# Performance work log

Hardware: AMD Instinct MI355X
Metric: run time of the kernel (lower is better)

## Reference

```python
import jax, jax.numpy as jnp
import numpy as np
from jax.scipy.special import gammaln

NPTS = 100          # hardcoded npts default in the torch module
EPS = 1e-8          # self.epsilon


def _build_grid(K):
    # Static quadrature grids for thresholds t_i = i/K, i=0..K.
    # Original code builds torch.linspace(eps, t_i - eps, int(NPTS * t_i)) per bin;
    # we precompute all K+1 grids padded to NPTS points with a validity mask.
    # (Note: the repo's thresholds arange/K*2-1 in [-1,1] crash torch.linspace for
    # negative b; we use the intended [0,1] Beta support thresholds t_i = i/K.)
    grid = np.full((K + 1, NPTS), 0.5, dtype=np.float32)  # 0.5 pad avoids log(0)
    mask = np.zeros((K + 1, NPTS), dtype=np.float32)
    for i in range(K + 1):
        n = int(NPTS * (i / K))
        if n > 0:
            grid[i, :n] = np.linspace(EPS, i / K - EPS, n, dtype=np.float32)
            mask[i, :n] = 1.0
    return jnp.asarray(grid), jnp.asarray(mask)


def setup_inputs() -> dict:
    key = jax.random.key(0)
    k1, k2, k3 = jax.random.split(key, 3)
    B, C, K = 65536, 512, 10
    x = jax.random.normal(k1, (B, C), dtype=jnp.float32)
    Wa = jax.random.normal(k2, (C, 1), dtype=jnp.float32) / np.sqrt(C)
    ba = jnp.zeros((1,), dtype=jnp.float32)
    Wb = jax.random.normal(k3, (C, 1), dtype=jnp.float32) / np.sqrt(C)
    bb = jnp.zeros((1,), dtype=jnp.float32)
    return {"x": x, "Wa": Wa, "ba": ba, "Wb": Wb, "bb": bb, "num_classes": K}


def reference(x, Wa, ba, Wb, bb, num_classes):
    K = int(num_classes)
    grid, mask = _build_grid(K)                      # [K+1, NPTS]
    # alpha/beta heads: Linear -> Softplus -> 1 + . -> clamp(1, 100)
    alpha = jnp.clip(1.0 + jax.nn.softplus(x @ Wa + ba), 1.0, 100.0)  # [B, 1]
    beta = jnp.clip(1.0 + jax.nn.softplus(x @ Wb + bb), 1.0, 100.0)   # [B, 1]
    a = alpha[:, :, None]                            # [B, 1, 1]
    b = beta[:, :, None]
    # Beta log_prob on all quadrature points: [B, K+1, NPTS]
    log_norm = gammaln(a) + gammaln(b) - gammaln(a + b)
    logpdf = (a - 1.0) * jnp.log(grid) + (b - 1.0) * jnp.log1p(-grid) - log_norm
    dx = 1.0 / (NPTS * K)                            # dx constant from original code
    cdf = jnp.sum(jnp.exp(logpdf) * mask, axis=-1) * dx   # [B, K+1] unnormalized CDFs
    probs = cdf[:, 1:] - cdf[:, :-1]                 # per-bin mass, [B, K]
    # diag(1/rowsum) @ probs  ==  row-normalize
    return probs / jnp.sum(probs, axis=-1, keepdims=True)
```

## Files before the change

kernel.cpp:

```cpp
#include <hip/hip_runtime.h>
#include <math.h>

#define NPTS_C 100
#define EPS_C 1e-8

#if defined(__has_builtin)
# if __has_builtin(__builtin_amdgcn_exp2f)
#  define FAST_EXP2(x) __builtin_amdgcn_exp2f(x)
#  define FAST_LOG2(x) __builtin_amdgcn_logf(x)
# else
#  define FAST_EXP2(x) exp2f(x)
#  define FAST_LOG2(x) log2f(x)
# endif
#else
# define FAST_EXP2(x) exp2f(x)
# define FAST_LOG2(x) log2f(x)
#endif

#define LOG2E_F 1.44269504088896340736f
#define LN2_F   0.69314718055994530942f

__device__ __forceinline__ float dot4(float4 a, float4 b) {
    return a.x * b.x + a.y * b.y + a.z * b.z + a.w * b.w;
}

__device__ __forceinline__ float wave_reduce_sum(float v) {
#pragma unroll
    for (int m = 1; m < 64; m <<= 1)
        v += __shfl_xor(v, m, 64);
    return v;
}

constexpr int KC   = 10;
constexpr int NTAB = 550;

__global__ __launch_bounds__(256, 6) void fused512_kernel(
    const float* __restrict__ x, const float* __restrict__ Wa,
    const float* __restrict__ ba, const float* __restrict__ Wb,
    const float* __restrict__ bb, float* __restrict__ out)
{
    __shared__ __align__(16) float2 s_tab[NTAB];
    __shared__ __align__(16) float4 s_w4[256];

    const int tid = threadIdx.x;

    if (tid < 128) {
        s_w4[tid]       = reinterpret_cast<const float4*>(Wa)[tid];
        s_w4[128 + tid] = reinterpret_cast<const float4*>(Wb)[tid];
    }

    {
        int base = 0;
#pragma unroll
        for (int i = 1; i <= KC; ++i) {
            const int n = 10 * i;
            const double start = EPS_C;
            const double stop  = (double)i / (double)KC - EPS_C;
            const double step  = (stop - start) / (double)(n - 1);
            for (int j = tid; j < n; j += 256) {
                const double g = (j == n - 1) ? stop : start + step * (double)j;
                const float g32 = (float)g;
                s_tab[base + j] = make_float2(log2f(g32), log2f(1.0f - g32));
            }
            base += n;
        }
    }
    __syncthreads();

    const int lane = tid & 63;
    const int wv   = tid >> 6;
    const int r8   = lane & 7;
    const int part = lane >> 3;
    const float ba0 = ba[0], bb0 = bb[0];

    const int row = blockIdx.x * 32 + wv * 8 + r8;
    const float* px = x + (size_t)row * 512 + part * 4;

    float da = 0.f, db = 0.f, da2 = 0.f, db2 = 0.f;
#pragma unroll
    for (int j = 0; j < 16; j += 2) {
        const float4 x0 = *reinterpret_cast<const float4*>(px + (size_t)j * 32);
        const float4 x1 = *reinterpret_cast<const float4*>(px + (size_t)(j + 1) * 32);
        da  += dot4(x0, s_w4[part + 8 * j]);
        db  += dot4(x0, s_w4[128 + part + 8 * j]);
        da2 += dot4(x1, s_w4[part + 8 * (j + 1)]);
        db2 += dot4(x1, s_w4[128 + part + 8 * (j + 1)]);
    }
    da += da2; db += db2;

    da += __shfl_xor(da, 8, 64);  db += __shfl_xor(db, 8, 64);
    da += __shfl_xor(da, 16, 64); db += __shfl_xor(db, 16, 64);
    da += __shfl_xor(da, 32, 64); db += __shfl_xor(db, 32, 64);
    da += ba0; db += bb0;

    const float ua = FAST_EXP2(-fabsf(da) * LOG2E_F);
    const float ub = FAST_EXP2(-fabsf(db) * LOG2E_F);
    const float sa = fmaxf(da, 0.f) + FAST_LOG2(1.f + ua) * LN2_F;
    const float sb = fmaxf(db, 0.f) + FAST_LOG2(1.f + ub) * LN2_F;
    const float alpha = fminf(fmaxf(1.f + sa, 1.f), 100.f);
    const float beta  = fminf(fmaxf(1.f + sb, 1.f), 100.f);
    const float am1 = alpha - 1.f, bm1 = beta - 1.f;

    const float den = am1 + bm1;
    float mm = (den > 0.f) ? am1 / den : 0.5f;
    mm = fminf(fmaxf(mm, 1e-6f), 1.f - 1e-6f);
    const float M2 = am1 * FAST_LOG2(mm) + bm1 * FAST_LOG2(1.f - mm);

    float seg[KC];
    {
        int base = 0;
#pragma unroll
        for (int i = 1; i <= KC; ++i) {
            const int n = 10 * i;
            float s = 0.f;
#pragma unroll
            for (int t = part; t < n; t += 8) {
                const float2 e = s_tab[base + t];
                s += FAST_EXP2(fmaf(am1, e.x, fmaf(bm1, e.y, -M2)));
            }
            seg[i - 1] = s;
            base += n;
        }
    }
#pragma unroll
    for (int i = 0; i < KC; ++i) {
        seg[i] += __shfl_xor(seg[i], 8, 64);
        seg[i] += __shfl_xor(seg[i], 16, 64);
        seg[i] += __shfl_xor(seg[i], 32, 64);
    }

    if (part == 0) {
        float* orow = out + (size_t)row * KC;
        const float inv_total = 1.f / seg[KC - 1];
        float prev = 0.f;
        float2* o2 = reinterpret_cast<float2*>(orow);
#pragma unroll
        for (int j = 0; j < KC; j += 2) {
            const float p0 = (seg[j]     - prev)   * inv_total;
            const float p1 = (seg[j + 1] - seg[j]) * inv_total;
            o2[j >> 1] = make_float2(p0, p1);
            prev = seg[j + 1];
        }
    }
}

__global__ __launch_bounds__(256, 4) void ub_fused_kernel(
    const float* __restrict__ x, const float* __restrict__ Wa,
    const float* __restrict__ ba, const float* __restrict__ Wb,
    const float* __restrict__ bb, float* __restrict__ out,
    int B, int C, int K)
{
    __shared__ __align__(16) float s_lg[600];
    __shared__ __align__(16) float s_l1g[600];
    __shared__ __align__(16) float s_w[1024];

    const int tid = threadIdx.x;
    for (int c = tid; c < C; c += blockDim.x) {
        s_w[c]     = Wa[c];
        s_w[C + c] = Wb[c];
    }
    {
        int base = 0;
        for (int i = 1; i <= K; ++i) {
            const int n = (int)((double)NPTS_C * ((double)i / (double)K));
            const double start = EPS_C;
            const double stop  = (double)i / (double)K - EPS_C;
            const double step  = (n > 1) ? (stop - start) / (double)(n - 1) : 0.0;
            for (int j = tid; j < n; j += blockDim.x) {
                float g = (j == n - 1) ? (float)stop : (float)(start + step * (double)j);
                s_lg[base + j]  = logf(g);
                s_l1g[base + j] = log1pf(-g);
            }
            base += n;
        }
    }
    __syncthreads();

    const float ba0 = ba[0], bb0 = bb[0];
    const int wave = tid >> 6;
    const int lane = tid & 63;
    const int wavesPerBlock = blockDim.x >> 6;
    const int waveId = blockIdx.x * wavesPerBlock + wave;
    const int nWaves = gridDim.x * wavesPerBlock;

    for (int row = waveId; row < B; row += nWaves) {
        const float* xr = x + (size_t)row * C;
        float da = 0.f, db = 0.f;
        for (int c0 = 0; c0 < C; c0 += 256) {
            const float4 xv = *reinterpret_cast<const float4*>(xr + c0 + 4 * lane);
            const float4 wa = *reinterpret_cast<const float4*>(&s_w[c0 + 4 * lane]);
            const float4 wb = *reinterpret_cast<const float4*>(&s_w[C + c0 + 4 * lane]);
            da += xv.x * wa.x + xv.y * wa.y + xv.z * wa.z + xv.w * wa.w;
            db += xv.x * wb.x + xv.y * wb.y + xv.z * wb.z + xv.w * wb.w;
        }
        da = wave_reduce_sum(da) + ba0;
        db = wave_reduce_sum(db) + bb0;

        const float sa = fmaxf(da, 0.f) + log1pf(expf(-fabsf(da)));
        const float sb = fmaxf(db, 0.f) + log1pf(expf(-fabsf(db)));
        const float alpha = fminf(fmaxf(1.f + sa, 1.f), 100.f);
        const float beta  = fminf(fmaxf(1.f + sb, 1.f), 100.f);
        const float log_norm = lgammaf(alpha) + lgammaf(beta) - lgammaf(alpha + beta);
        const float am1 = alpha - 1.f, bm1 = beta - 1.f;

        float cdf_prev = 0.f, myp = 0.f;
        int base = 0;
        for (int i = 1; i <= K; ++i) {
            const int n = (int)((double)NPTS_C * ((double)i / (double)K));
            float s = 0.f;
            for (int p = lane; p < n; p += 64) {
                const float lp = fmaf(am1, s_lg[base + p],
                                 fmaf(bm1, s_l1g[base + p], -log_norm));
                s += expf(lp);
            }
            const float cdf = wave_reduce_sum(s);
            if (lane == i - 1) myp = cdf - cdf_prev;
            cdf_prev = cdf;
            base += n;
        }
        if (lane < K)
            out[(size_t)row * K + lane] = myp / cdf_prev;
    }
}

extern "C" void kernel_launch(void* const* d_in, const int* in_sizes, int n_in,
                              void* d_out, int out_size, void* d_ws, size_t ws_size,
                              hipStream_t stream) {
    const float* x  = (const float*)d_in[0];
    const float* Wa = (const float*)d_in[1];
    const float* ba = (const float*)d_in[2];
    const float* Wb = (const float*)d_in[3];
    const float* bb = (const float*)d_in[4];
    float* out = (float*)d_out;

    const int C = in_sizes[1];
    const int B = in_sizes[0] / C;
    const int K = out_size / B;

    const bool fast_ok = (C == 512) && (K == 10) && (B % 32 == 0);

    if (fast_ok) {
        fused512_kernel<<<B / 32, 256, 0, stream>>>(x, Wa, ba, Wb, bb, out);
    } else {
        int nblocks = (B + 3) / 4;
        if (nblocks > 2048) nblocks = 2048;
        ub_fused_kernel<<<nblocks, 256, 0, stream>>>(x, Wa, ba, Wb, bb, out, B, C, K);
    }
}
```

Before: 33.91 us.

## Coalesce row loads per wave and hold weight slices in registers

Each wave now reads its 8 rows as one contiguous span, so every 64-lane float4 load covers 1 KB of consecutive memory instead of eight scattered 128-byte pieces. The Wa/Wb weights are loaded straight from global memory into per-lane registers, which removes the shared-memory weight table and its LDS reads. The mismatch between this load layout and one-row-per-lane ownership is handled by 48 extra cross-lane shuffles plus per-lane selects to route partial sums back to each row's lanes. The 16 float4 values now held in registers per thread raise register pressure, so the launch-bounds occupancy hint drops from 6 to 4 blocks.

```diff
diff --git a/kernel.cpp b/kernel.cpp
--- a/kernel.cpp
+++ b/kernel.cpp
@@ -34,20 +34,14 @@
 constexpr int KC   = 10;
 constexpr int NTAB = 550;
 
-__global__ __launch_bounds__(256, 6) void fused512_kernel(
+__global__ __launch_bounds__(256, 4) void fused512_kernel(
     const float* __restrict__ x, const float* __restrict__ Wa,
     const float* __restrict__ ba, const float* __restrict__ Wb,
     const float* __restrict__ bb, float* __restrict__ out)
 {
     __shared__ __align__(16) float2 s_tab[NTAB];
-    __shared__ __align__(16) float4 s_w4[256];
 
     const int tid = threadIdx.x;
-
-    if (tid < 128) {
-        s_w4[tid]       = reinterpret_cast<const float4*>(Wa)[tid];
-        s_w4[128 + tid] = reinterpret_cast<const float4*>(Wb)[tid];
-    }
 
     {
         int base = 0;
@@ -73,21 +67,42 @@
     const int part = lane >> 3;
     const float ba0 = ba[0], bb0 = bb[0];
 
-    const int row = blockIdx.x * 32 + wv * 8 + r8;
-    const float* px = x + (size_t)row * 512 + part * 4;
-
-    float da = 0.f, db = 0.f, da2 = 0.f, db2 = 0.f;
-#pragma unroll
-    for (int j = 0; j < 16; j += 2) {
-        const float4 x0 = *reinterpret_cast<const float4*>(px + (size_t)j * 32);
-        const float4 x1 = *reinterpret_cast<const float4*>(px + (size_t)(j + 1) * 32);
-        da  += dot4(x0, s_w4[part + 8 * j]);
-        db  += dot4(x0, s_w4[128 + part + 8 * j]);
-        da2 += dot4(x1, s_w4[part + 8 * (j + 1)]);
-        db2 += dot4(x1, s_w4[128 + part + 8 * (j + 1)]);
-    }
-    da += da2; db += db2;
-
+    const float4* Wa4 = reinterpret_cast<const float4*>(Wa);
+    const float4* Wb4 = reinterpret_cast<const float4*>(Wb);
+    const float4 wa_lo = Wa4[lane], wa_hi = Wa4[64 + lane];
+    const float4 wb_lo = Wb4[lane], wb_hi = Wb4[64 + lane];
+
+    const int row0 = blockIdx.x * 32 + wv * 8;
+    const float4* px = reinterpret_cast<const float4*>(x) + (size_t)row0 * 128 + lane;
+
+    float4 xv[16];
+#pragma unroll
+    for (int j = 0; j < 16; ++j)
+        xv[j] = px[j * 64];
+
+    float acca[8], accb[8];
+#pragma unroll
+    for (int r = 0; r < 8; ++r) {
+        acca[r] = dot4(xv[2 * r], wa_lo) + dot4(xv[2 * r + 1], wa_hi);
+        accb[r] = dot4(xv[2 * r], wb_lo) + dot4(xv[2 * r + 1], wb_hi);
+    }
+
+#pragma unroll
+    for (int r = 0; r < 8; ++r) {
+        acca[r] += __shfl_xor(acca[r], 1, 64);
+        accb[r] += __shfl_xor(accb[r], 1, 64);
+        acca[r] += __shfl_xor(acca[r], 2, 64);
+        accb[r] += __shfl_xor(accb[r], 2, 64);
+        acca[r] += __shfl_xor(acca[r], 4, 64);
+        accb[r] += __shfl_xor(accb[r], 4, 64);
+    }
+    float da = acca[0], db = accb[0];
+#pragma unroll
+    for (int r = 1; r < 8; ++r) {
+        const bool sel = (r8 == r);
+        da = sel ? acca[r] : da;
+        db = sel ? accb[r] : db;
+    }
     da += __shfl_xor(da, 8, 64);  db += __shfl_xor(db, 8, 64);
     da += __shfl_xor(da, 16, 64); db += __shfl_xor(db, 16, 64);
     da += __shfl_xor(da, 32, 64); db += __shfl_xor(db, 32, 64);
@@ -130,7 +145,7 @@
     }
 
     if (part == 0) {
-        float* orow = out + (size_t)row * KC;
+        float* orow = out + (size_t)(row0 + r8) * KC;
         const float inv_total = 1.f / seg[KC - 1];
         float prev = 0.f;
         float2* o2 = reinterpret_cast<float2*>(orow);
```

Result: faster. 29.98 us (median of 5 runs) (-11.6%).
